# Performance work log

Hardware: AMD Instinct MI355X
Metric: run time of the kernel (lower is better)

## Reference

```python
import jax, jax.numpy as jnp
import numpy as np

N_NODES, N_EDGES, N_FEAT, N_CLASSES = 100000, 1600000, 50, 40
K_HOPS = 2


def setup_inputs() -> dict:
    key = jax.random.key(0)
    k1, k2, k3 = jax.random.split(key, 3)
    x = jax.random.normal(k1, (N_NODES, N_FEAT), dtype=jnp.float32)
    edge_index = jax.random.randint(k2, (2, N_EDGES), 0, N_NODES, dtype=jnp.int64)
    # Linear(num_features -> num_classes) params (PyG stores [out,in]; we use [in,out])
    W = jax.random.normal(k3, (N_FEAT, N_CLASSES), dtype=jnp.float32) * 0.05
    b = jnp.zeros((N_CLASSES,), dtype=jnp.float32)
    return {"x": x, "edge_index": edge_index, "W": W, "b": b}


def reference(x, edge_index, W, b):
    N = x.shape[0]
    # gcn_norm: add self-loops, symmetric normalization D^-1/2 (A+I) D^-1/2
    loop = jnp.arange(N, dtype=edge_index.dtype)
    row = jnp.concatenate([edge_index[0], loop])  # source nodes
    col = jnp.concatenate([edge_index[1], loop])  # target nodes
    deg = jax.ops.segment_sum(jnp.ones(row.shape[0], x.dtype), col, num_segments=N)
    deg_inv_sqrt = jnp.where(deg > 0, jax.lax.rsqrt(deg), 0.0)
    norm = deg_inv_sqrt[row] * deg_inv_sqrt[col]  # [E+N]

    # K-hop propagation: h <- scatter_add(norm * h[row] -> col)
    h = x
    for _ in range(K_HOPS):
        h = jax.ops.segment_sum(norm[:, None] * h[row], col, num_segments=N)

    logits = h @ W + b  # [N, C]
    return jax.nn.log_softmax(logits, axis=1)
```

## Files before the change

### kernel.cpp

```cpp
#include <hip/hip_runtime.h>
#include <hip/hip_fp16.h>
#include <math.h>

#define NFEAT 50
#define NCLS 40
#define TPBK 256
#define TPBK_SHIFT 8
#define EPB 4096
#define MAXNB 512
#define CAP 8192

__device__ __forceinline__ __half2 u2h2(unsigned u) { return *(__half2*)&u; }
__device__ __forceinline__ unsigned h22u(__half2 h) { return *(unsigned*)&h; }
__device__ __forceinline__ __half2 shx_h2(__half2 v, int m) {
    int i = *(int*)&v; i = __shfl_xor(i, m); return *(__half2*)&i;
}


__global__ __launch_bounds__(1024) void k_bhist(const int* __restrict__ col, int E,
                                                int* __restrict__ hist, int NB) {
    __shared__ int h[MAXNB];
    for (int i = threadIdx.x; i < NB; i += 1024) h[i] = 0;
    __syncthreads();
    int i0 = blockIdx.x * EPB;
    #pragma unroll
    for (int k = 0; k < EPB / 1024; k++) {
        int e = i0 + k * 1024 + threadIdx.x;
        if (e < E) atomicAdd(&h[col[e] >> TPBK_SHIFT], 1);
    }
    __syncthreads();
    int* row = hist + (size_t)blockIdx.x * NB;
    for (int i = threadIdx.x; i < NB; i += 1024) row[i] = h[i];
}


__global__ __launch_bounds__(1024) void k_colscan(int* __restrict__ hist,
                                                  int* __restrict__ btot,
                                                  int NB, int PE) {
    int b = (blockIdx.x * 1024 + threadIdx.x) >> 6;
    int lane = threadIdx.x & 63;
    if (b >= NB) return;
    int carry = b * CAP;
    for (int c = 0; c < PE; c += 64) {
        int p = c + lane;
        int v = (p < PE) ? hist[(size_t)p * NB + b] : 0;
        int incl = v;
        #pragma unroll
        for (int d = 1; d < 64; d <<= 1) {
            int tmp = __shfl_up(incl, d);
            if (lane >= d) incl += tmp;
        }
        if (p < PE) hist[(size_t)p * NB + b] = carry + incl - v;
        carry += __shfl(incl, 63);
    }
    if (lane == 0) btot[b] = carry - b * CAP;
}


__global__ __launch_bounds__(1024) void k_part(const int* __restrict__ ei, int E,
                                               const int* __restrict__ hist,
                                               unsigned* __restrict__ pairs, int NB) {
    __shared__ int h[MAXNB];
    __shared__ int base[MAXNB];
    int t = threadIdx.x;
    const int* brow = hist + (size_t)blockIdx.x * NB;
    for (int i = t; i < NB; i += 1024) { h[i] = 0; base[i] = brow[i]; }
    __syncthreads();
    int i0 = blockIdx.x * EPB;
    int r[EPB / 1024], c[EPB / 1024];
    #pragma unroll
    for (int k = 0; k < EPB / 1024; k++) {
        int e = i0 + k * 1024 + t;
        if (e < E) {
            r[k] = ei[e];
            c[k] = ei[E + e];
        } else c[k] = -1;
    }
    #pragma unroll
    for (int k = 0; k < EPB / 1024; k++) {
        if (c[k] >= 0) {
            int bkt = c[k] >> TPBK_SHIFT;
            int p = base[bkt] + atomicAdd(&h[bkt], 1);
            pairs[p] = ((unsigned)r[k] << 8) | ((unsigned)c[k] & 255u);
        }
    }
}


__global__ __launch_bounds__(1024) void k_bucket(const unsigned* __restrict__ pairs,
                         const int* __restrict__ btot, int* __restrict__ rows,
                         int* __restrict__ cnt, int* __restrict__ offs,
                         float* __restrict__ dis, const float* __restrict__ x,
                         unsigned short* __restrict__ xb, int N) {
    int b = blockIdx.x;
    int ebeg = b * CAP, m = btot[b];
    int t0 = b << TPBK_SHIFT;
    __shared__ int h[TPBK];
    __shared__ int off[TPBK];
    __shared__ float diss[TPBK];
    __shared__ int wtot[4];
    int t = threadIdx.x;
    if (t < TPBK) h[t] = 0;
    __syncthreads();

    unsigned pc[4]; bool ok[4];
    #pragma unroll
    for (int k = 0; k < 4; k++) {
        int i = t + k * 1024;
        ok[k] = i < m;
        if (ok[k]) {
            pc[k] = pairs[ebeg + i];
            atomicAdd(&h[pc[k] & 255u], 1);
        }
    }
    for (int i = 4096 + t; i < m; i += 1024)
        atomicAdd(&h[pairs[ebeg + i] & 255u], 1);
    __syncthreads();

    int v = 0, incl = 0;
    if (t < TPBK) {
        v = h[t];
        h[t] = 0;
        incl = v;
        int l = t & 63;
        #pragma unroll
        for (int d = 1; d < 64; d <<= 1) {
            int tmp = __shfl_up(incl, d);
            if (l >= d) incl += tmp;
        }
        if (l == 63) wtot[t >> 6] = incl;
    }
    __syncthreads();
    if (t < TPBK) {
        int pre = 0;
        #pragma unroll
        for (int w = 0; w < 3; w++) if ((t >> 6) > w) pre += wtot[w];
        int excl = pre + incl - v;
        off[t] = excl;
        int tg = t0 + t;
        float d = rsqrtf((float)(v + 1));
        diss[t] = d;
        if (tg < N) {
            cnt[tg] = v;
            offs[tg] = ebeg + excl;
            dis[tg] = d;
        }
    }
    __syncthreads();

    #pragma unroll
    for (int k = 0; k < 4; k++) {
        if (ok[k]) {
            int lt = pc[k] & 255u;
            int pos = off[lt] + atomicAdd(&h[lt], 1);
            rows[ebeg + pos] = pc[k] >> 8;
        }
    }
    for (int i = 4096 + t; i < m; i += 1024) {
        unsigned p = pairs[ebeg + i];
        int lt = p & 255u;
        int pos = off[lt] + atomicAdd(&h[lt], 1);
        rows[ebeg + pos] = p >> 8;
    }

    int nmax = N - t0; if (nmax > TPBK) nmax = TPBK;
    for (int idx = t; idx < (nmax << 6); idx += 1024) {
        int nl = idx >> 6, f = idx & 63;
        int n = t0 + nl;
        float val = (f < NFEAT) ? x[(size_t)n * NFEAT + f] * diss[nl] : 0.f;
        __half hv = __float2half_rn(val);
        xb[((size_t)n << 6) + f] = *(unsigned short*)&hv;
    }
}


__global__ void k_prop(const unsigned short* __restrict__ zin, unsigned short* __restrict__ zout,
                       const float* __restrict__ dis, const int* __restrict__ offs,
                       const int* __restrict__ cnt, const int* __restrict__ rows, int N) {
    int wid = (blockIdx.x * blockDim.x + threadIdx.x) >> 6;
    int lane = threadIdx.x & 63;
    if (wid >= N) return;
    int g = lane >> 3;
    unsigned fl = (lane & 7) << 3;
    int beg = offs[wid], num = cnt[wid];

    uint4 sv = *(const uint4*)&zin[((unsigned)wid << 6) + fl];
    __half2 a0 = u2h2(g == 0 ? sv.x : 0u);
    __half2 a1 = u2h2(g == 0 ? sv.y : 0u);
    __half2 a2 = u2h2(g == 0 ? sv.z : 0u);
    __half2 a3 = u2h2(g == 0 ? sv.w : 0u);

    int full = num & ~31;
    int j = 0;
    for (; j < full; j += 32) {
        unsigned i0 = (unsigned)(beg + j) + (unsigned)g;
        int r0 = rows[i0], r1 = rows[i0 + 8], r2 = rows[i0 + 16], r3 = rows[i0 + 24];
        uint4 v0 = *(const uint4*)&zin[((unsigned)r0 << 6) + fl];
        uint4 v1 = *(const uint4*)&zin[((unsigned)r1 << 6) + fl];
        uint4 v2 = *(const uint4*)&zin[((unsigned)r2 << 6) + fl];
        uint4 v3 = *(const uint4*)&zin[((unsigned)r3 << 6) + fl];
        a0 = __hadd2(a0, __hadd2(__hadd2(u2h2(v0.x), u2h2(v1.x)),
                                 __hadd2(u2h2(v2.x), u2h2(v3.x))));
        a1 = __hadd2(a1, __hadd2(__hadd2(u2h2(v0.y), u2h2(v1.y)),
                                 __hadd2(u2h2(v2.y), u2h2(v3.y))));
        a2 = __hadd2(a2, __hadd2(__hadd2(u2h2(v0.z), u2h2(v1.z)),
                                 __hadd2(u2h2(v2.z), u2h2(v3.z))));
        a3 = __hadd2(a3, __hadd2(__hadd2(u2h2(v0.w), u2h2(v1.w)),
                                 __hadd2(u2h2(v2.w), u2h2(v3.w))));
    }
    if (j < num) {
        int e0 = j + g, e1 = e0 + 8, e2 = e0 + 16, e3 = e0 + 24;
        int c0 = e0 < num ? e0 : 0;
        int c1 = e1 < num ? e1 : 0;
        int c2 = e2 < num ? e2 : 0;
        int c3 = e3 < num ? e3 : 0;
        int r0 = rows[beg + c0];
        int r1 = rows[beg + c1];
        int r2 = rows[beg + c2];
        int r3 = rows[beg + c3];
        uint4 v0 = *(const uint4*)&zin[((unsigned)r0 << 6) + fl];
        uint4 v1 = *(const uint4*)&zin[((unsigned)r1 << 6) + fl];
        uint4 v2 = *(const uint4*)&zin[((unsigned)r2 << 6) + fl];
        uint4 v3 = *(const uint4*)&zin[((unsigned)r3 << 6) + fl];
        if (e0 >= num) { v0.x = 0u; v0.y = 0u; v0.z = 0u; v0.w = 0u; }
        if (e1 >= num) { v1.x = 0u; v1.y = 0u; v1.z = 0u; v1.w = 0u; }
        if (e2 >= num) { v2.x = 0u; v2.y = 0u; v2.z = 0u; v2.w = 0u; }
        if (e3 >= num) { v3.x = 0u; v3.y = 0u; v3.z = 0u; v3.w = 0u; }
        a0 = __hadd2(a0, __hadd2(__hadd2(u2h2(v0.x), u2h2(v1.x)),
                                 __hadd2(u2h2(v2.x), u2h2(v3.x))));
        a1 = __hadd2(a1, __hadd2(__hadd2(u2h2(v0.y), u2h2(v1.y)),
                                 __hadd2(u2h2(v2.y), u2h2(v3.y))));
        a2 = __hadd2(a2, __hadd2(__hadd2(u2h2(v0.z), u2h2(v1.z)),
                                 __hadd2(u2h2(v2.z), u2h2(v3.z))));
        a3 = __hadd2(a3, __hadd2(__hadd2(u2h2(v0.w), u2h2(v1.w)),
                                 __hadd2(u2h2(v2.w), u2h2(v3.w))));
    }

    a0 = __hadd2(a0, shx_h2(a0, 8)); a0 = __hadd2(a0, shx_h2(a0, 16)); a0 = __hadd2(a0, shx_h2(a0, 32));
    a1 = __hadd2(a1, shx_h2(a1, 8)); a1 = __hadd2(a1, shx_h2(a1, 16)); a1 = __hadd2(a1, shx_h2(a1, 32));
    a2 = __hadd2(a2, shx_h2(a2, 8)); a2 = __hadd2(a2, shx_h2(a2, 16)); a2 = __hadd2(a2, shx_h2(a2, 32));
    a3 = __hadd2(a3, shx_h2(a3, 8)); a3 = __hadd2(a3, shx_h2(a3, 16)); a3 = __hadd2(a3, shx_h2(a3, 32));

    if (lane < 8) {
        float dn = dis[wid];
        float s2 = dn * dn;
        float2 f0 = __half22float2(a0);
        float2 f1 = __half22float2(a1);
        float2 f2 = __half22float2(a2);
        float2 f3 = __half22float2(a3);
        uint4 o;
        o.x = h22u(__floats2half2_rn(f0.x * s2, f0.y * s2));
        o.y = h22u(__floats2half2_rn(f1.x * s2, f1.y * s2));
        o.z = h22u(__floats2half2_rn(f2.x * s2, f2.y * s2));
        o.w = h22u(__floats2half2_rn(f3.x * s2, f3.y * s2));
        *(uint4*)&zout[((unsigned)wid << 6) + fl] = o;
    }
}


__global__ __launch_bounds__(256) void k_head(const unsigned short* __restrict__ z2,
                       const int* __restrict__ cnt,
                       const float* __restrict__ W, const float* __restrict__ b,
                       float* __restrict__ out, int N) {
    __shared__ float Ws[NFEAT * NCLS];
    __shared__ float bs[NCLS];
    int t = threadIdx.x;
    for (int i = t; i < NFEAT * NCLS / 4; i += 256)
        *(float4*)&Ws[i * 4] = *(const float4*)&W[i * 4];
    if (t < NCLS) bs[t] = b[t];
    __syncthreads();

    int tid = blockIdx.x * 256 + t;
    int n = tid >> 3;
    int l = tid & 7;
    if (n >= N) return;

    float acc0 = 0.f, acc1 = 0.f, acc2 = 0.f, acc3 = 0.f, acc4 = 0.f;
    const unsigned* zr = (const unsigned*)&z2[(size_t)n << 6];
    int cb = l * 5;
    #pragma unroll
    for (int k2 = 0; k2 < NFEAT / 2; k2++) {
        float2 hp = __half22float2(u2h2(zr[k2]));
        const float* w0 = &Ws[(2 * k2) * NCLS + cb];
        const float* w1 = &Ws[(2 * k2 + 1) * NCLS + cb];
        acc0 += hp.x * w0[0] + hp.y * w1[0];
        acc1 += hp.x * w0[1] + hp.y * w1[1];
        acc2 += hp.x * w0[2] + hp.y * w1[2];
        acc3 += hp.x * w0[3] + hp.y * w1[3];
        acc4 += hp.x * w0[4] + hp.y * w1[4];
    }
    float s = sqrtf((float)(cnt[n] + 1));
    float l0 = s * acc0 + bs[cb + 0];
    float l1 = s * acc1 + bs[cb + 1];
    float l2 = s * acc2 + bs[cb + 2];
    float l3 = s * acc3 + bs[cb + 3];
    float l4 = s * acc4 + bs[cb + 4];

    float m = fmaxf(fmaxf(fmaxf(l0, l1), fmaxf(l2, l3)), l4);
    m = fmaxf(m, __shfl_xor(m, 1));
    m = fmaxf(m, __shfl_xor(m, 2));
    m = fmaxf(m, __shfl_xor(m, 4));
    float sum = __expf(l0 - m) + __expf(l1 - m) + __expf(l2 - m)
              + __expf(l3 - m) + __expf(l4 - m);
    sum += __shfl_xor(sum, 1);
    sum += __shfl_xor(sum, 2);
    sum += __shfl_xor(sum, 4);
    float lse = __logf(sum) + m;

    float* o = &out[(size_t)n * NCLS + cb];
    o[0] = l0 - lse; o[1] = l1 - lse; o[2] = l2 - lse;
    o[3] = l3 - lse; o[4] = l4 - lse;
}


extern "C" void kernel_launch(void* const* d_in, const int* in_sizes, int n_in,
                              void* d_out, int out_size, void* d_ws, size_t ws_size,
                              hipStream_t stream) {
    const float* x = (const float*)d_in[0];
    const int* ei = (const int*)d_in[1];
    const float* W = (const float*)d_in[2];
    const float* b = (const float*)d_in[3];
    float* out = (float*)d_out;

    int N = in_sizes[0] / NFEAT;
    int E = in_sizes[1] / 2;
    int NB = (N + TPBK - 1) / TPBK;
    int pe = (E + EPB - 1) / EPB;

    char* w = (char*)d_ws;
    auto alloc = [&](size_t bytes) { char* p = w; w += (bytes + 255) & ~(size_t)255; return p; };
    int*   hist  = (int*)  alloc((size_t)pe * NB * 4);
    int*   btot  = (int*)  alloc((size_t)NB * 4);
    int*   cnt   = (int*)  alloc((size_t)N * 4);
    int*   offs  = (int*)  alloc((size_t)N * 4);
    float* dis   = (float*)alloc((size_t)N * 4);
    int*   rows  = (int*)  alloc((size_t)NB * CAP * 4);
    unsigned short* xb = (unsigned short*)alloc((size_t)N * 64 * 2);
    unsigned short* z1 = (unsigned short*)alloc((size_t)N * 64 * 2);
    size_t psz = (size_t)NB * CAP * 4, zsz = (size_t)N * 64 * 2;
    char* uni = alloc(psz > zsz ? psz : zsz);
    unsigned* pairs = (unsigned*)uni;
    unsigned short* z2 = (unsigned short*)uni;

    k_bhist<<<pe, 1024, 0, stream>>>(ei + E, E, hist, NB);
    int cb = (NB * 64 + 1023) / 1024;
    k_colscan<<<cb, 1024, 0, stream>>>(hist, btot, NB, pe);
    k_part<<<pe, 1024, 0, stream>>>(ei, E, hist, pairs, NB);
    k_bucket<<<NB, 1024, 0, stream>>>(pairs, btot, rows, cnt, offs, dis, x, xb, N);

    int pb = (int)(((size_t)N * 64 + 255) / 256);
    k_prop<<<pb, 256, 0, stream>>>(xb, z1, dis, offs, cnt, rows, N);
    k_prop<<<pb, 256, 0, stream>>>(z1, z2, dis, offs, cnt, rows, N);

    int hb = (int)(((size_t)N * 8 + 255) / 256);
    k_head<<<hb, 256, 0, stream>>>(z2, cnt, W, b, out, N);
}
```

Before: 137.8 us.

## Replace histogram+scan bucketing with single-pass atomic bucket reservation

```diff
diff --git a/kernel.cpp b/kernel.cpp
--- a/kernel.cpp
+++ b/kernel.cpp
@@ -6,7 +6,7 @@
 #define NCLS 40
 #define TPBK 256
 #define TPBK_SHIFT 8
-#define EPB 4096
+#define EPB 16384
 #define MAXNB 512
 #define CAP 8192
 
@@ -17,54 +17,19 @@
 }
 
 
-__global__ __launch_bounds__(1024) void k_bhist(const int* __restrict__ col, int E,
-                                                int* __restrict__ hist, int NB) {
-    __shared__ int h[MAXNB];
-    for (int i = threadIdx.x; i < NB; i += 1024) h[i] = 0;
-    __syncthreads();
-    int i0 = blockIdx.x * EPB;
-    #pragma unroll
-    for (int k = 0; k < EPB / 1024; k++) {
-        int e = i0 + k * 1024 + threadIdx.x;
-        if (e < E) atomicAdd(&h[col[e] >> TPBK_SHIFT], 1);
-    }
-    __syncthreads();
-    int* row = hist + (size_t)blockIdx.x * NB;
-    for (int i = threadIdx.x; i < NB; i += 1024) row[i] = h[i];
-}
-
-
-__global__ __launch_bounds__(1024) void k_colscan(int* __restrict__ hist,
-                                                  int* __restrict__ btot,
-                                                  int NB, int PE) {
-    int b = (blockIdx.x * 1024 + threadIdx.x) >> 6;
-    int lane = threadIdx.x & 63;
-    if (b >= NB) return;
-    int carry = b * CAP;
-    for (int c = 0; c < PE; c += 64) {
-        int p = c + lane;
-        int v = (p < PE) ? hist[(size_t)p * NB + b] : 0;
-        int incl = v;
-        #pragma unroll
-        for (int d = 1; d < 64; d <<= 1) {
-            int tmp = __shfl_up(incl, d);
-            if (lane >= d) incl += tmp;
-        }
-        if (p < PE) hist[(size_t)p * NB + b] = carry + incl - v;
-        carry += __shfl(incl, 63);
-    }
-    if (lane == 0) btot[b] = carry - b * CAP;
-}
-
-
-__global__ __launch_bounds__(1024) void k_part(const int* __restrict__ ei, int E,
-                                               const int* __restrict__ hist,
-                                               unsigned* __restrict__ pairs, int NB) {
+__global__ void k_init(int* __restrict__ gcur, int NB) {
+    int b = blockIdx.x * 256 + threadIdx.x;
+    if (b < NB) gcur[b] = b * CAP;
+}
+
+
+__global__ __launch_bounds__(1024) void k_partall(const int* __restrict__ ei, int E,
+                                                  int* __restrict__ gcur,
+                                                  unsigned* __restrict__ pairs, int NB) {
     __shared__ int h[MAXNB];
     __shared__ int base[MAXNB];
     int t = threadIdx.x;
-    const int* brow = hist + (size_t)blockIdx.x * NB;
-    for (int i = t; i < NB; i += 1024) { h[i] = 0; base[i] = brow[i]; }
+    for (int i = t; i < NB; i += 1024) h[i] = 0;
     __syncthreads();
     int i0 = blockIdx.x * EPB;
     int r[EPB / 1024], c[EPB / 1024];
@@ -74,8 +39,15 @@
         if (e < E) {
             r[k] = ei[e];
             c[k] = ei[E + e];
+            atomicAdd(&h[c[k] >> TPBK_SHIFT], 1);
         } else c[k] = -1;
     }
+    __syncthreads();
+    for (int i = t; i < NB; i += 1024)
+        base[i] = h[i] ? atomicAdd(&gcur[i], h[i]) : 0;
+    __syncthreads();
+    for (int i = t; i < NB; i += 1024) h[i] = 0;
+    __syncthreads();
     #pragma unroll
     for (int k = 0; k < EPB / 1024; k++) {
         if (c[k] >= 0) {
@@ -88,12 +60,13 @@
 
 
 __global__ __launch_bounds__(1024) void k_bucket(const unsigned* __restrict__ pairs,
-                         const int* __restrict__ btot, int* __restrict__ rows,
+                         const int* __restrict__ gcur, int* __restrict__ rows,
                          int* __restrict__ cnt, int* __restrict__ offs,
                          float* __restrict__ dis, const float* __restrict__ x,
                          unsigned short* __restrict__ xb, int N) {
     int b = blockIdx.x;
-    int ebeg = b * CAP, m = btot[b];
+    int ebeg = b * CAP;
+    int m = gcur[b] - ebeg;
     int t0 = b << TPBK_SHIFT;
     __shared__ int h[TPBK];
     __shared__ int off[TPBK];
@@ -174,10 +147,11 @@
 }
 
 
-__global__ void k_prop(const unsigned short* __restrict__ zin, unsigned short* __restrict__ zout,
+__global__ __launch_bounds__(512) void k_prop(const unsigned short* __restrict__ zin,
+                       unsigned short* __restrict__ zout,
                        const float* __restrict__ dis, const int* __restrict__ offs,
                        const int* __restrict__ cnt, const int* __restrict__ rows, int N) {
-    int wid = (blockIdx.x * blockDim.x + threadIdx.x) >> 6;
+    int wid = (blockIdx.x * 512 + threadIdx.x) >> 6;
     int lane = threadIdx.x & 63;
     if (wid >= N) return;
     int g = lane >> 3;
@@ -210,14 +184,11 @@
     }
     if (j < num) {
         int e0 = j + g, e1 = e0 + 8, e2 = e0 + 16, e3 = e0 + 24;
-        int c0 = e0 < num ? e0 : 0;
-        int c1 = e1 < num ? e1 : 0;
-        int c2 = e2 < num ? e2 : 0;
-        int c3 = e3 < num ? e3 : 0;
-        int r0 = rows[beg + c0];
-        int r1 = rows[beg + c1];
-        int r2 = rows[beg + c2];
-        int r3 = rows[beg + c3];
+        int r0 = 0, r1 = 0, r2 = 0, r3 = 0;
+        if (e0 < num) r0 = rows[beg + e0];
+        if (e1 < num) r1 = rows[beg + e1];
+        if (e2 < num) r2 = rows[beg + e2];
+        if (e3 < num) r3 = rows[beg + e3];
         uint4 v0 = *(const uint4*)&zin[((unsigned)r0 << 6) + fl];
         uint4 v1 = *(const uint4*)&zin[((unsigned)r1 << 6) + fl];
         uint4 v2 = *(const uint4*)&zin[((unsigned)r2 << 6) + fl];
@@ -329,8 +300,7 @@
 
     char* w = (char*)d_ws;
     auto alloc = [&](size_t bytes) { char* p = w; w += (bytes + 255) & ~(size_t)255; return p; };
-    int*   hist  = (int*)  alloc((size_t)pe * NB * 4);
-    int*   btot  = (int*)  alloc((size_t)NB * 4);
+    int*   gcur  = (int*)  alloc((size_t)NB * 4);
     int*   cnt   = (int*)  alloc((size_t)N * 4);
     int*   offs  = (int*)  alloc((size_t)N * 4);
     float* dis   = (float*)alloc((size_t)N * 4);
@@ -342,15 +312,13 @@
     unsigned* pairs = (unsigned*)uni;
     unsigned short* z2 = (unsigned short*)uni;
 
-    k_bhist<<<pe, 1024, 0, stream>>>(ei + E, E, hist, NB);
-    int cb = (NB * 64 + 1023) / 1024;
-    k_colscan<<<cb, 1024, 0, stream>>>(hist, btot, NB, pe);
-    k_part<<<pe, 1024, 0, stream>>>(ei, E, hist, pairs, NB);
-    k_bucket<<<NB, 1024, 0, stream>>>(pairs, btot, rows, cnt, offs, dis, x, xb, N);
-
-    int pb = (int)(((size_t)N * 64 + 255) / 256);
-    k_prop<<<pb, 256, 0, stream>>>(xb, z1, dis, offs, cnt, rows, N);
-    k_prop<<<pb, 256, 0, stream>>>(z1, z2, dis, offs, cnt, rows, N);
+    k_init<<<(NB + 255) / 256, 256, 0, stream>>>(gcur, NB);
+    k_partall<<<pe, 1024, 0, stream>>>(ei, E, gcur, pairs, NB);
+    k_bucket<<<NB, 1024, 0, stream>>>(pairs, gcur, rows, cnt, offs, dis, x, xb, N);
+
+    int pb = (int)(((size_t)N * 64 + 511) / 512);
+    k_prop<<<pb, 512, 0, stream>>>(xb, z1, dis, offs, cnt, rows, N);
+    k_prop<<<pb, 512, 0, stream>>>(z1, z2, dis, offs, cnt, rows, N);
 
     int hb = (int)(((size_t)N * 8 + 255) / 256);
     k_head<<<hb, 256, 0, stream>>>(z2, cnt, W, b, out, N);
```

Result: slower. 146.9 us (+6.6%).
